# Performance work log

Hardware: AMD Instinct MI355X
Metric: run time of the kernel (lower is better)

The kernel has to match this reference:

```python
import jax, jax.numpy as jnp
import numpy as np

REVIEW_RATIO = 0.3  # init kwarg


def setup_inputs() -> dict:
    key = jax.random.key(0)
    k1, k2 = jax.random.split(key)
    N, C = 32768, 1000
    output = jax.random.normal(k1, (N, C), dtype=jnp.float32)
    target = jax.random.randint(k2, (N,), 0, C, dtype=jnp.int64)
    return {"output": output, "target": target}


def reference(output, target):
    # per-sample cross-entropy: -log_softmax(output)[i, target[i]]
    logp = jax.nn.log_softmax(output, axis=-1)               # [N, C]
    ce = -jnp.take_along_axis(logp, target[:, None], axis=-1)[:, 0]  # [N]
    n = ce.shape[0]
    k = int(n * REVIEW_RATIO)
    # descending sort; threshold is the k-th largest loss
    sorted_desc = jnp.sort(ce)[::-1]
    lam = sorted_desc[k]
    # zero out losses strictly below the threshold, then mean over ALL samples
    kept = jnp.where(ce < lam, jnp.zeros_like(ce), ce)
    return kept.mean()
```

## Files before the change

kernel.cpp:

```cpp
#include <hip/hip_runtime.h>
#include <stdint.h>


typedef unsigned int uint32;

__global__ __launch_bounds__(256) void ce_kernel(
    const float* __restrict__ logits, const int* __restrict__ target,
    float* __restrict__ ce, int N, int C) {
  const int lane = (int)(threadIdx.x & 63);
  const int row = (int)((blockIdx.x * blockDim.x + threadIdx.x) >> 6);
  if (row >= N) return;

  const float* rp = logits + (size_t)row * (size_t)C;

  const int t = target[row];
  const float ot = rp[t];

  const float4* rp4 = (const float4*)rp;
  const int nv4 = C >> 2;
  const float4 NEG = make_float4(-INFINITY, -INFINITY, -INFINITY, -INFINITY);

  float4 v0 = (lane       < nv4) ? rp4[lane      ] : NEG;
  float4 v1 = (lane +  64 < nv4) ? rp4[lane +  64] : NEG;
  float4 v2 = (lane + 128 < nv4) ? rp4[lane + 128] : NEG;
  float4 v3 = (lane + 192 < nv4) ? rp4[lane + 192] : NEG;

  float m = fmaxf(fmaxf(fmaxf(v0.x, v0.y), fmaxf(v0.z, v0.w)),
                  fmaxf(fmaxf(fmaxf(v1.x, v1.y), fmaxf(v1.z, v1.w)),
                        fmaxf(fmaxf(fmaxf(v2.x, v2.y), fmaxf(v2.z, v2.w)),
                              fmaxf(fmaxf(v3.x, v3.y), fmaxf(v3.z, v3.w)))));
#pragma unroll
  for (int off = 1; off < 64; off <<= 1) m = fmaxf(m, __shfl_xor(m, off));

  float e = __expf(v0.x - m) + __expf(v0.y - m) + __expf(v0.z - m) + __expf(v0.w - m)
          + __expf(v1.x - m) + __expf(v1.y - m) + __expf(v1.z - m) + __expf(v1.w - m)
          + __expf(v2.x - m) + __expf(v2.y - m) + __expf(v2.z - m) + __expf(v2.w - m)
          + __expf(v3.x - m) + __expf(v3.y - m) + __expf(v3.z - m) + __expf(v3.w - m);
#pragma unroll
  for (int off = 1; off < 64; off <<= 1) e += __shfl_xor(e, off);

  if (lane == 0) {
    float cev = (m - ot) + __logf(e);
    ce[row] = fmaxf(cev, 0.0f);
  }
}

__device__ __forceinline__ uint32 bin_count(const uint32* h, uint32 b) {
  uint32 w = h[b >> 1];
  return (b & 1u) ? (w >> 16) : (w & 0xFFFFu);
}

__global__ __launch_bounds__(1024) void select_kernel(
    const float* __restrict__ ce, float* __restrict__ out, int N, int k) {
  __shared__ uint32 h[8192];
  __shared__ uint32 g[1024];
  __shared__ uint32 sel[4];
  __shared__ uint32 candcnt;
  __shared__ double wsum[16];
  const int tid = (int)threadIdx.x;
  const float4* ce4 = (const float4*)ce;
  const int N4 = N >> 2;
  const uint32 kk = (uint32)k;

#pragma unroll
  for (int j = 0; j < 8; ++j) h[tid + 1024 * j] = 0;
  __syncthreads();

  for (int i = tid; i < N4; i += 1024) {
    float4 x = ce4[i];
    uint32 k0 = __float_as_uint(x.x) >> 17;
    uint32 k1 = __float_as_uint(x.y) >> 17;
    uint32 k2 = __float_as_uint(x.z) >> 17;
    uint32 k3 = __float_as_uint(x.w) >> 17;
    atomicAdd(&h[k0 >> 1], (k0 & 1u) ? 0x10000u : 1u);
    atomicAdd(&h[k1 >> 1], (k1 & 1u) ? 0x10000u : 1u);
    atomicAdd(&h[k2 >> 1], (k2 & 1u) ? 0x10000u : 1u);
    atomicAdd(&h[k3 >> 1], (k3 & 1u) ? 0x10000u : 1u);
  }
  __syncthreads();

  {
    uint32 c = 0;
#pragma unroll
    for (int j = 0; j < 8; ++j) {
      uint32 w = h[8 * tid + j];
      c += (w & 0xFFFFu) + (w >> 16);
    }
    g[tid] = c;
  }
  __syncthreads();

  for (int off = 1; off < 1024; off <<= 1) {
    uint32 val = g[tid] + ((tid + off < 1024) ? g[tid + off] : 0u);
    __syncthreads();
    g[tid] = val;
    __syncthreads();
  }

  {
    uint32 SG = (tid + 1 < 1024) ? g[tid + 1] : 0u;
    if (SG <= kk && kk < g[tid]) { sel[0] = (uint32)tid; sel[1] = kk - SG; }
  }
  __syncthreads();

  if (tid == 0) {
    uint32 grp = sel[0];
    uint32 kg = sel[1];
    uint32 acc = 0;
    for (int b = 15; b >= 0; --b) {
      uint32 bin = grp * 16u + (uint32)b;
      uint32 c = bin_count(h, bin);
      if (kg < acc + c) { sel[0] = bin; sel[1] = kg - acc; break; }
      acc += c;
    }
    candcnt = 0;
  }
  __syncthreads();
  const uint32 K = sel[0];
  const uint32 kprime = sel[1];
  __syncthreads();

  double acc = 0.0;
  for (int i = tid; i < N4; i += 1024) {
    float4 x = ce4[i];
    uint32 u0 = __float_as_uint(x.x), u1 = __float_as_uint(x.y);
    uint32 u2 = __float_as_uint(x.z), u3 = __float_as_uint(x.w);
    if ((u0 >> 17) > K) acc += (double)x.x;
    else if ((u0 >> 17) == K) { uint32 p = atomicAdd(&candcnt, 1u); if (p < 8192u) h[p] = u0; }
    if ((u1 >> 17) > K) acc += (double)x.y;
    else if ((u1 >> 17) == K) { uint32 p = atomicAdd(&candcnt, 1u); if (p < 8192u) h[p] = u1; }
    if ((u2 >> 17) > K) acc += (double)x.z;
    else if ((u2 >> 17) == K) { uint32 p = atomicAdd(&candcnt, 1u); if (p < 8192u) h[p] = u2; }
    if ((u3 >> 17) > K) acc += (double)x.w;
    else if ((u3 >> 17) == K) { uint32 p = atomicAdd(&candcnt, 1u); if (p < 8192u) h[p] = u3; }
  }
  __syncthreads();

  const uint32 c = (candcnt < 8192u) ? candcnt : 8192u;
  for (uint32 j = (uint32)tid; j < c; j += 1024u) {
    uint32 uj = h[j];
    uint32 grt = 0, eq = 0;
    for (uint32 l = 0; l < c; ++l) {
      uint32 v = h[l];
      grt += (v > uj) ? 1u : 0u;
      eq += (v == uj) ? 1u : 0u;
    }
    if (grt <= kprime && kprime < grt + eq) sel[2] = uj;
  }
  __syncthreads();
  const uint32 lam_u = sel[2];

  for (uint32 j = (uint32)tid; j < c; j += 1024u) {
    uint32 uj = h[j];
    if (uj >= lam_u) acc += (double)__uint_as_float(uj);
  }

#pragma unroll
  for (int off = 1; off < 64; off <<= 1) acc += __shfl_xor(acc, off);
  if ((tid & 63) == 0) wsum[tid >> 6] = acc;
  __syncthreads();
  if (tid == 0) {
    double tsum = 0.0;
    for (int i = 0; i < 16; ++i) tsum += wsum[i];
    out[0] = (float)(tsum / (double)N);
  }
}

extern "C" void kernel_launch(void* const* d_in, const int* in_sizes, int n_in,
                              void* d_out, int out_size, void* d_ws, size_t ws_size,
                              hipStream_t stream) {
  const float* logits = (const float*)d_in[0];
  const int* target = (const int*)d_in[1];
  float* out = (float*)d_out;

  const int N = in_sizes[1];
  const int C = in_sizes[0] / N;

  float* ce = (float*)d_ws;

  int grid = (N + 3) / 4;
  ce_kernel<<<grid, 256, 0, stream>>>(logits, target, ce, N, C);

  int k = (int)((double)N * 0.3);

  select_kernel<<<1, 1024, 0, stream>>>(ce, out, N, k);
}
```

Before: 214.2 us.

## Fuse CE histogram into CE kernel and replace quadratic candidate rank with radix passes

The first-level histogram is now built inside the cross-entropy kernel, in per-block shared memory. It is flushed into 8 replicated global histograms, so the single-block select kernel no longer makes its own histogram pass over the losses. The select kernel replaces the O(c^2) pairwise ranking of threshold candidates with a second 14-bit histogram level plus a 16-bin final level. It also uses wave-aggregated atomics for candidate compaction. In exchange it adds a memset launch, per-block 32KB LDS histograms that lower occupancy in the CE kernel, and global atomics to flush histograms.

Result: slower. 224.0 us (+4.6%).

```diff
diff --git a/kernel.cpp b/kernel.cpp
--- a/kernel.cpp
+++ b/kernel.cpp
@@ -4,154 +4,196 @@
 
 typedef unsigned int uint32;
 
-__global__ __launch_bounds__(256) void ce_kernel(
+
+__global__ __launch_bounds__(256) void ce_hist_kernel(
     const float* __restrict__ logits, const int* __restrict__ target,
-    float* __restrict__ ce, int N, int C) {
-  const int lane = (int)(threadIdx.x & 63);
-  const int row = (int)((blockIdx.x * blockDim.x + threadIdx.x) >> 6);
-  if (row >= N) return;
-
-  const float* rp = logits + (size_t)row * (size_t)C;
-
-  const int t = target[row];
-  const float ot = rp[t];
-
-  const float4* rp4 = (const float4*)rp;
+    float* __restrict__ ce, uint32* __restrict__ ghist, int N, int C) {
+  __shared__ uint32 lh[8192];
+  const int tid = (int)threadIdx.x;
+  const int lane = tid & 63;
+  const int wid = tid >> 6;
+
+  for (int j = tid; j < 8192; j += 256) lh[j] = 0;
+  __syncthreads();
+
+  const float4 NEG = make_float4(-INFINITY, -INFINITY, -INFINITY, -INFINITY);
   const int nv4 = C >> 2;
-  const float4 NEG = make_float4(-INFINITY, -INFINITY, -INFINITY, -INFINITY);
-
-  float4 v0 = (lane       < nv4) ? rp4[lane      ] : NEG;
-  float4 v1 = (lane +  64 < nv4) ? rp4[lane +  64] : NEG;
-  float4 v2 = (lane + 128 < nv4) ? rp4[lane + 128] : NEG;
-  float4 v3 = (lane + 192 < nv4) ? rp4[lane + 192] : NEG;
-
-  float m = fmaxf(fmaxf(fmaxf(v0.x, v0.y), fmaxf(v0.z, v0.w)),
-                  fmaxf(fmaxf(fmaxf(v1.x, v1.y), fmaxf(v1.z, v1.w)),
-                        fmaxf(fmaxf(fmaxf(v2.x, v2.y), fmaxf(v2.z, v2.w)),
-                              fmaxf(fmaxf(v3.x, v3.y), fmaxf(v3.z, v3.w)))));
-#pragma unroll
-  for (int off = 1; off < 64; off <<= 1) m = fmaxf(m, __shfl_xor(m, off));
-
-  float e = __expf(v0.x - m) + __expf(v0.y - m) + __expf(v0.z - m) + __expf(v0.w - m)
-          + __expf(v1.x - m) + __expf(v1.y - m) + __expf(v1.z - m) + __expf(v1.w - m)
-          + __expf(v2.x - m) + __expf(v2.y - m) + __expf(v2.z - m) + __expf(v2.w - m)
-          + __expf(v3.x - m) + __expf(v3.y - m) + __expf(v3.z - m) + __expf(v3.w - m);
-#pragma unroll
-  for (int off = 1; off < 64; off <<= 1) e += __shfl_xor(e, off);
-
-  if (lane == 0) {
-    float cev = (m - ot) + __logf(e);
-    ce[row] = fmaxf(cev, 0.0f);
-  }
-}
-
-__device__ __forceinline__ uint32 bin_count(const uint32* h, uint32 b) {
-  uint32 w = h[b >> 1];
-  return (b & 1u) ? (w >> 16) : (w & 0xFFFFu);
+  const int rbase = (int)blockIdx.x * 64 + wid * 16;
+
+  for (int r = 0; r < 16; ++r) {
+    const int row = rbase + r;
+    if (row >= N) break;
+    const float* rp = logits + (size_t)row * (size_t)C;
+
+    const int t = target[row];
+    const float ot = rp[t];
+
+    const float4* rp4 = (const float4*)rp;
+    float4 v0 = (lane       < nv4) ? rp4[lane      ] : NEG;
+    float4 v1 = (lane +  64 < nv4) ? rp4[lane +  64] : NEG;
+    float4 v2 = (lane + 128 < nv4) ? rp4[lane + 128] : NEG;
+    float4 v3 = (lane + 192 < nv4) ? rp4[lane + 192] : NEG;
+
+    float m = fmaxf(fmaxf(fmaxf(v0.x, v0.y), fmaxf(v0.z, v0.w)),
+                    fmaxf(fmaxf(fmaxf(v1.x, v1.y), fmaxf(v1.z, v1.w)),
+                          fmaxf(fmaxf(fmaxf(v2.x, v2.y), fmaxf(v2.z, v2.w)),
+                                fmaxf(fmaxf(v3.x, v3.y), fmaxf(v3.z, v3.w)))));
+#pragma unroll
+    for (int off = 1; off < 64; off <<= 1) m = fmaxf(m, __shfl_xor(m, off));
+
+    float e = __expf(v0.x - m) + __expf(v0.y - m) + __expf(v0.z - m) + __expf(v0.w - m)
+            + __expf(v1.x - m) + __expf(v1.y - m) + __expf(v1.z - m) + __expf(v1.w - m)
+            + __expf(v2.x - m) + __expf(v2.y - m) + __expf(v2.z - m) + __expf(v2.w - m)
+            + __expf(v3.x - m) + __expf(v3.y - m) + __expf(v3.z - m) + __expf(v3.w - m);
+#pragma unroll
+    for (int off = 1; off < 64; off <<= 1) e += __shfl_xor(e, off);
+
+    if (lane == 0) {
+      float cev = fmaxf((m - ot) + __logf(e), 0.0f);
+      ce[row] = cev;
+      uint32 key = __float_as_uint(cev) >> 17;
+      atomicAdd(&lh[key >> 1], (key & 1u) ? 0x10000u : 1u);
+    }
+  }
+  __syncthreads();
+
+  uint32* gh = ghist + (size_t)(blockIdx.x & 7) * 8192;
+  for (int j = tid; j < 8192; j += 256) {
+    uint32 w = lh[j];
+    if (w) atomicAdd(&gh[j], w);
+  }
+}
+
+
+__device__ void find_level(uint32* H, uint32* g, uint32 rank, int tid,
+                           volatile uint32* sel) {
+  uint32 c = 0;
+#pragma unroll
+  for (int j = 0; j < 8; ++j) {
+    uint32 w = H[8 * tid + j];
+    c += (w & 0xFFFFu) + (w >> 16);
+  }
+  g[tid] = c;
+  __syncthreads();
+  for (int off = 1; off < 1024; off <<= 1) {
+    uint32 v = g[tid] + ((tid + off < 1024) ? g[tid + off] : 0u);
+    __syncthreads();
+    g[tid] = v;
+    __syncthreads();
+  }
+  uint32 SG = (tid + 1 < 1024) ? g[tid + 1] : 0u;
+  if (SG <= rank && rank < g[tid]) { sel[0] = (uint32)tid; sel[1] = rank - SG; }
+  __syncthreads();
+  if (tid == 0) {
+    uint32 grp = sel[0], kg = sel[1], acc = 0;
+    for (int b = 15; b >= 0; --b) {
+      uint32 bin = grp * 16u + (uint32)b;
+      uint32 w = H[bin >> 1];
+      uint32 cc = (bin & 1u) ? (w >> 16) : (w & 0xFFFFu);
+      if (kg < acc + cc) { sel[0] = bin; sel[1] = kg - acc; break; }
+      acc += cc;
+    }
+  }
+  __syncthreads();
 }
 
 __global__ __launch_bounds__(1024) void select_kernel(
-    const float* __restrict__ ce, float* __restrict__ out, int N, int k) {
-  __shared__ uint32 h[8192];
+    const float* __restrict__ ce, const uint32* __restrict__ ghist,
+    float* __restrict__ out, int N, int k) {
+  __shared__ uint32 H[8192];
+  __shared__ uint32 Cand[8192];
   __shared__ uint32 g[1024];
-  __shared__ uint32 sel[4];
-  __shared__ uint32 candcnt;
+  __shared__ uint32 sel[2];
+  __shared__ uint32 ccnt;
+  __shared__ uint32 cnt16[16];
   __shared__ double wsum[16];
   const int tid = (int)threadIdx.x;
+  const int lane = tid & 63;
   const float4* ce4 = (const float4*)ce;
   const int N4 = N >> 2;
-  const uint32 kk = (uint32)k;
-
-#pragma unroll
-  for (int j = 0; j < 8; ++j) h[tid + 1024 * j] = 0;
-  __syncthreads();
-
-  for (int i = tid; i < N4; i += 1024) {
-    float4 x = ce4[i];
-    uint32 k0 = __float_as_uint(x.x) >> 17;
-    uint32 k1 = __float_as_uint(x.y) >> 17;
-    uint32 k2 = __float_as_uint(x.z) >> 17;
-    uint32 k3 = __float_as_uint(x.w) >> 17;
-    atomicAdd(&h[k0 >> 1], (k0 & 1u) ? 0x10000u : 1u);
-    atomicAdd(&h[k1 >> 1], (k1 & 1u) ? 0x10000u : 1u);
-    atomicAdd(&h[k2 >> 1], (k2 & 1u) ? 0x10000u : 1u);
-    atomicAdd(&h[k3 >> 1], (k3 & 1u) ? 0x10000u : 1u);
-  }
-  __syncthreads();
-
-  {
-    uint32 c = 0;
-#pragma unroll
-    for (int j = 0; j < 8; ++j) {
-      uint32 w = h[8 * tid + j];
-      c += (w & 0xFFFFu) + (w >> 16);
-    }
-    g[tid] = c;
-  }
-  __syncthreads();
-
-  for (int off = 1; off < 1024; off <<= 1) {
-    uint32 val = g[tid] + ((tid + off < 1024) ? g[tid + off] : 0u);
-    __syncthreads();
-    g[tid] = val;
-    __syncthreads();
-  }
-
-  {
-    uint32 SG = (tid + 1 < 1024) ? g[tid + 1] : 0u;
-    if (SG <= kk && kk < g[tid]) { sel[0] = (uint32)tid; sel[1] = kk - SG; }
-  }
-  __syncthreads();
-
+
+  if (tid == 0) ccnt = 0;
+  if (tid < 16) cnt16[tid] = 0;
+
+  for (int j = tid; j < 8192; j += 1024) {
+    uint32 w = 0;
+#pragma unroll
+    for (int r = 0; r < 8; ++r) w += ghist[(size_t)r * 8192 + j];
+    H[j] = w;
+  }
+  __syncthreads();
+
+  find_level(H, g, (uint32)k, tid, sel);
+  const uint32 K = sel[0];
+  const uint32 kr1 = sel[1];
+  __syncthreads();
+
+  double acc = 0.0;
+  const int iters = (N4 + 1023) / 1024;
+  for (int it = 0; it < iters; ++it) {
+    int i = it * 1024 + tid;
+    float4 x;
+    if (i < N4) x = ce4[i];
+    else x = make_float4(-1.0f, -1.0f, -1.0f, -1.0f);
+    bool valid = (i < N4);
+    uint32 u[4];
+    float f[4];
+    f[0] = x.x; f[1] = x.y; f[2] = x.z; f[3] = x.w;
+#pragma unroll
+    for (int j = 0; j < 4; ++j) {
+      u[j] = __float_as_uint(f[j]);
+      uint32 key = u[j] >> 17;
+      if (valid && key > K) acc += (double)f[j];
+      bool mine = valid && (key == K);
+      unsigned long long mk = __ballot(mine);
+      uint32 cnt = (uint32)__popcll(mk);
+      if (cnt) {
+        int src = (int)__ffsll(mk) - 1;
+        uint32 base = 0;
+        if (lane == src) base = atomicAdd(&ccnt, cnt);
+        base = (uint32)__shfl((int)base, src);
+        if (mine) {
+          uint32 p = base + (uint32)__popcll(mk & ((1ull << lane) - 1ull));
+          if (p < 8192u) Cand[p] = u[j];
+        }
+      }
+    }
+  }
+  __syncthreads();
+  const uint32 c = (ccnt < 8192u) ? ccnt : 8192u;
+
+  for (int j = tid; j < 8192; j += 1024) H[j] = 0;
+  __syncthreads();
+  for (uint32 j = (uint32)tid; j < c; j += 1024u) {
+    uint32 key2 = (Cand[j] >> 4) & 0x3FFFu;
+    atomicAdd(&H[key2 >> 1], (key2 & 1u) ? 0x10000u : 1u);
+  }
+  __syncthreads();
+  find_level(H, g, kr1, tid, sel);
+  const uint32 B2 = sel[0];
+  const uint32 kr2 = sel[1];
+  __syncthreads();
+
+  const uint32 lam_hi = (K << 17) | (B2 << 4);
+
+  for (uint32 j = (uint32)tid; j < c; j += 1024u) {
+    uint32 uj = Cand[j];
+    if ((uj >> 4) == (lam_hi >> 4)) atomicAdd(&cnt16[uj & 15u], 1u);
+  }
+  __syncthreads();
   if (tid == 0) {
-    uint32 grp = sel[0];
-    uint32 kg = sel[1];
-    uint32 acc = 0;
+    uint32 kg = kr2, accu = 0;
     for (int b = 15; b >= 0; --b) {
-      uint32 bin = grp * 16u + (uint32)b;
-      uint32 c = bin_count(h, bin);
-      if (kg < acc + c) { sel[0] = bin; sel[1] = kg - acc; break; }
-      acc += c;
-    }
-    candcnt = 0;
-  }
-  __syncthreads();
-  const uint32 K = sel[0];
-  const uint32 kprime = sel[1];
-  __syncthreads();
-
-  double acc = 0.0;
-  for (int i = tid; i < N4; i += 1024) {
-    float4 x = ce4[i];
-    uint32 u0 = __float_as_uint(x.x), u1 = __float_as_uint(x.y);
-    uint32 u2 = __float_as_uint(x.z), u3 = __float_as_uint(x.w);
-    if ((u0 >> 17) > K) acc += (double)x.x;
-    else if ((u0 >> 17) == K) { uint32 p = atomicAdd(&candcnt, 1u); if (p < 8192u) h[p] = u0; }
-    if ((u1 >> 17) > K) acc += (double)x.y;
-    else if ((u1 >> 17) == K) { uint32 p = atomicAdd(&candcnt, 1u); if (p < 8192u) h[p] = u1; }
-    if ((u2 >> 17) > K) acc += (double)x.z;
-    else if ((u2 >> 17) == K) { uint32 p = atomicAdd(&candcnt, 1u); if (p < 8192u) h[p] = u2; }
-    if ((u3 >> 17) > K) acc += (double)x.w;
-    else if ((u3 >> 17) == K) { uint32 p = atomicAdd(&candcnt, 1u); if (p < 8192u) h[p] = u3; }
-  }
-  __syncthreads();
-
-  const uint32 c = (candcnt < 8192u) ? candcnt : 8192u;
+      uint32 cc = cnt16[b];
+      if (kg < accu + cc) { sel[0] = lam_hi | (uint32)b; break; }
+      accu += cc;
+    }
+  }
+  __syncthreads();
+  const uint32 lam_u = sel[0];
+
   for (uint32 j = (uint32)tid; j < c; j += 1024u) {
-    uint32 uj = h[j];
-    uint32 grt = 0, eq = 0;
-    for (uint32 l = 0; l < c; ++l) {
-      uint32 v = h[l];
-      grt += (v > uj) ? 1u : 0u;
-      eq += (v == uj) ? 1u : 0u;
-    }
-    if (grt <= kprime && kprime < grt + eq) sel[2] = uj;
-  }
-  __syncthreads();
-  const uint32 lam_u = sel[2];
-
-  for (uint32 j = (uint32)tid; j < c; j += 1024u) {
-    uint32 uj = h[j];
+    uint32 uj = Cand[j];
     if (uj >= lam_u) acc += (double)__uint_as_float(uj);
   }
 
@@ -177,11 +219,14 @@
   const int C = in_sizes[0] / N;
 
   float* ce = (float*)d_ws;
-
-  int grid = (N + 3) / 4;
-  ce_kernel<<<grid, 256, 0, stream>>>(logits, target, ce, N, C);
+  uint32* ghist = (uint32*)((char*)d_ws + (size_t)N * sizeof(float));
+
+  hipMemsetAsync(ghist, 0, 8 * 8192 * sizeof(uint32), stream);
+
+  int grid = (N + 63) / 64;
+  ce_hist_kernel<<<grid, 256, 0, stream>>>(logits, target, ce, ghist, N, C);
 
   int k = (int)((double)N * 0.3);
 
-  select_kernel<<<1, 1024, 0, stream>>>(ce, out, N, k);
-}
+  select_kernel<<<1, 1024, 0, stream>>>(ce, ghist, out, N, k);
+}
```
